# Performance work log

Hardware: AMD Instinct MI355X
Metric: run time of the kernel (lower is better)

Reference implementation:

```python
import jax, jax.numpy as jnp
import numpy as np

E = 8          # node_emb_dim (number of LSTM ensembles)
H = 128        # fixed_lstm_hidden
D = 8          # feature dim
CONT = 168     # cont_len (encoder length)
HORIZON = 24   # decoder length
T = CONT + HORIZON
B = 4096       # batch of node ids
NUM_TS = 4096


def _lstm(xs, W, U, b, h0, c0):
    """Time-major LSTM (Keras gate order i,f,g,o). xs: [T,B,in]. Returns final (h,c) and all hs."""
    def step(carry, x):
        h, c = carry
        z = x @ W + h @ U + b                      # [B, 4H]
        i, f, g, o = jnp.split(z, 4, axis=-1)
        i = jax.nn.sigmoid(i)
        f = jax.nn.sigmoid(f)
        g = jnp.tanh(g)
        o = jax.nn.sigmoid(o)
        c = f * c + i * g
        h = o * jnp.tanh(c)
        return (h, c), h
    (h, c), hs = jax.lax.scan(step, (h0, c0), xs)
    return h, c, hs


def setup_inputs() -> dict:
    key = jax.random.key(0)
    ks = jax.random.split(key, 12)
    s = 0.05  # small init scale to keep LSTM gates unsaturated
    return {
        "feats": jax.random.normal(ks[0], (T, D), jnp.float32),
        "y_prev": jax.random.normal(ks[1], (CONT, B), jnp.float32),
        "nid": jax.random.randint(ks[2], (B,), 0, NUM_TS, jnp.int32),
        "emb_table": jax.random.uniform(ks[3], (NUM_TS, E), jnp.float32),
        "enc_W": jax.random.normal(ks[4], (E, 1 + D, 4 * H), jnp.float32) * s,
        "enc_U": jax.random.normal(ks[5], (E, H, 4 * H), jnp.float32) * s,
        "enc_b": jnp.zeros((E, 4 * H), jnp.float32),
        "dec_W": jax.random.normal(ks[6], (E, D, 4 * H), jnp.float32) * s,
        "dec_U": jax.random.normal(ks[7], (E, H, 4 * H), jnp.float32) * s,
        "dec_b": jnp.zeros((E, 4 * H), jnp.float32),
        "out_w": jax.random.normal(ks[8], (E, H), jnp.float32) * s,
    }


def reference(feats, y_prev, nid, emb_table, enc_W, enc_U, enc_b, dec_W, dec_U, dec_b, out_w):
    cont_len = y_prev.shape[0]
    b = nid.shape[0]
    # normalized node embedding: abs then row-normalize, then lookup
    embs = jnp.abs(emb_table)
    embs = embs / jnp.sum(embs, axis=1, keepdims=True)
    node_emb = embs[nid]                                   # [B, E]
    # broadcast features over batch (time-major)
    feats_b = jnp.broadcast_to(feats[:, None, :], (feats.shape[0], b, feats.shape[1]))
    enc_inp = jnp.concatenate([y_prev[..., None], feats_b[:cont_len]], axis=-1)  # [CONT,B,1+D]
    feats_futr = feats_b[cont_len:]                        # [HOR,B,D]
    hdim = enc_U.shape[1]
    h0 = jnp.zeros((b, hdim), feats.dtype)
    c0 = jnp.zeros((b, hdim), feats.dtype)

    def run_one(eW, eU, eb, dW, dU, db, ow):
        h, c, _ = _lstm(enc_inp, eW, eU, eb, h0, c0)
        _, _, hs = _lstm(feats_futr, dW, dU, db, h, c)     # [HOR,B,H]
        return jnp.einsum('tbh,h->tb', hs, ow)             # Dense(1, no bias) -> [HOR,B]

    outs = jax.vmap(run_one)(enc_W, enc_U, enc_b, dec_W, dec_U, dec_b, out_w)  # [E,HOR,B]
    fixed_effect = jnp.einsum('etb,be->tb', outs, node_emb)                    # [HOR,B]
    return fixed_effect
```

## Files before the change

kernel.cpp:

```cpp
#include <hip/hip_runtime.h>
#include <stdint.h>
#include <type_traits>

#define NE 8
#define NH 128
#define ND 8
#define NCONT 168
#define NHOR 24
#define NB 4096
#define NG 512
#define BT 64

#define S_SIG (-1.44269504088896f)
#define S_TANH (2.88539008177793f)

typedef float f32x4 __attribute__((ext_vector_type(4)));
typedef float f32x2 __attribute__((ext_vector_type(2)));
typedef short bf16x8 __attribute__((ext_vector_type(8)));
typedef unsigned int u32x2 __attribute__((ext_vector_type(2)));

template <int N> using ic = std::integral_constant<int, N>;

__device__ __forceinline__ unsigned short f2bf(float f){
  union { float f; unsigned u; } v; v.f = f;
  unsigned r = (v.u + 0x7FFFu + ((v.u >> 16) & 1u)) >> 16;
  return (unsigned short)r;
}
__device__ __forceinline__ unsigned cvt_pk_bf16(float lo, float hi){
  unsigned r;
  asm("v_cvt_pk_bf16_f32 %0, %1, %2" : "=v"(r) : "v"(lo), "v"(hi));
  return r;
}

__device__ __forceinline__ f32x2 splat2(float v){ f32x2 r; r.x = v; r.y = v; return r; }
__device__ __forceinline__ f32x2 lo2(f32x4 v){ return __builtin_shufflevector(v, v, 0, 1); }
__device__ __forceinline__ f32x2 hi2(f32x4 v){ return __builtin_shufflevector(v, v, 2, 3); }
__device__ __forceinline__ f32x2 fma2(f32x2 a, f32x2 b, f32x2 c){
  return __builtin_elementwise_fma(a, b, c);
}
__device__ __forceinline__ f32x2 exp2_2(f32x2 x){
  f32x2 o; o.x = __builtin_amdgcn_exp2f(x.x); o.y = __builtin_amdgcn_exp2f(x.y); return o;
}
__device__ __forceinline__ f32x2 rcp2(f32x2 x){
  f32x2 o; o.x = __builtin_amdgcn_rcpf(x.x); o.y = __builtin_amdgcn_rcpf(x.y); return o;
}
__device__ __forceinline__ f32x2 gate2(f32x2 zs){
  return rcp2(exp2_2(zs) + splat2(1.0f));
}

__global__ void prep_fxw_enc(const float* __restrict__ feats, const float* __restrict__ W,
                             const float* __restrict__ bias, float* __restrict__ out){
  int idx = blockIdx.x * blockDim.x + threadIdx.x;
  if (idx >= NE * NCONT * NG) return;
  int j = idx & (NG - 1);
  int t = (idx >> 9) % NCONT;
  int e = idx / (NCONT * NG);
  float s = bias[e * NG + j];
  #pragma unroll
  for (int i = 0; i < ND; ++i)
    s += feats[t * ND + i] * W[(e * 9 + 1 + i) * NG + j];
  float sc = ((j >> 7) == 2) ? S_TANH : S_SIG;
  out[idx] = s * sc;
}

__global__ void prep_fxw_dec(const float* __restrict__ feats, const float* __restrict__ W,
                             const float* __restrict__ bias, float* __restrict__ out){
  int idx = blockIdx.x * blockDim.x + threadIdx.x;
  if (idx >= NE * NHOR * NG) return;
  int j = idx & (NG - 1);
  int t = (idx >> 9) % NHOR;
  int e = idx / (NHOR * NG);
  float s = bias[e * NG + j];
  #pragma unroll
  for (int i = 0; i < ND; ++i)
    s += feats[(NCONT + t) * ND + i] * W[(e * ND + i) * NG + j];
  float sc = ((j >> 7) == 2) ? S_TANH : S_SIG;
  out[idx] = s * sc;
}

__global__ void prep_node(const int* __restrict__ nid, const float* __restrict__ emb,
                          float* __restrict__ node_w){
  int b = blockIdx.x * blockDim.x + threadIdx.x;
  if (b >= NB) return;
  int n = nid[b];
  float a[NE]; float s = 0.f;
  #pragma unroll
  for (int e = 0; e < NE; ++e){ a[e] = fabsf(emb[n * NE + e]); s += a[e]; }
  float inv = 1.0f / s;
  #pragma unroll
  for (int e = 0; e < NE; ++e) node_w[b * NE + e] = a[e] * inv;
}

__global__ __launch_bounds__(512, 2) void lstm_main(
    const float* __restrict__ y_prev,
    const float* __restrict__ enc_W,
    const float* __restrict__ enc_U,
    const float* __restrict__ dec_U,
    const float* __restrict__ out_w,
    const float* __restrict__ fxw_enc,
    const float* __restrict__ fxw_dec,
    float* __restrict__ ws_out)
{
  __shared__ unsigned short hl[2][BT * NH];
  __shared__ float part[2][BT][9];

  const int tid  = threadIdx.x;
  const int lane = tid & 63;
  const int w    = tid >> 6;
  const int e    = blockIdx.x & 7;
  const int b0   = (blockIdx.x >> 3) * BT;
  const int l15  = lane & 15;
  const int l4   = lane >> 4;
  const int hc0  = w * 16 + l4 * 4;

  const int q   = (l15 >> 2) & 1;
  const int Ae  = l15 * 128 + ((l4 ^ (l15 & 3)) << 3);
  const int rb0 = 2 * (Ae + q * 32);
  const int rb1 = 2 * (Ae + (1 - q) * 32);
  const int wb  = 2 * ((l15 * 128 + hc0) ^ ((l15 & 7) << 3));

  {
    f32x4 z4 = {0.f, 0.f, 0.f, 0.f};
    ((f32x4*)&hl[0][0])[tid]       = z4;
    ((f32x4*)&hl[0][0])[tid + 512] = z4;
  }

  bf16x8 ut[4][4];
  {
    const float* Ub = enc_U + e * NH * NG + w * 16 + l15;
    #pragma unroll
    for (int g = 0; g < 4; ++g){
      float scg = (g == 2) ? S_TANH : S_SIG;
      #pragma unroll
      for (int kc = 0; kc < 4; ++kc){
        const float* p = Ub + (kc * 32 + l4 * 8) * NG + g * NH;
        bf16x8 v;
        #pragma unroll
        for (int j = 0; j < 8; ++j) v[j] = (short)f2bf(p[j * NG] * scg);
        ut[g][kc] = v;
      }
    }
  }

  f32x2 w042[4][2];
  #pragma unroll
  for (int g = 0; g < 4; ++g){
    float scg = (g == 2) ? S_TANH : S_SIG;
    f32x4 t4 = *(const f32x4*)&enc_W[(e * 9) * NG + g * NH + hc0];
    t4 *= scg;
    w042[g][0] = lo2(t4); w042[g][1] = hi2(t4);
  }

  f32x2 cs2[4][2];
  #pragma unroll
  for (int nf = 0; nf < 4; ++nf){ cs2[nf][0] = splat2(0.f); cs2[nf][1] = splat2(0.f); }

  f32x2 ow2[2];
  f32x4 fxv[4];
  float yv[4];

  const float* fxe = fxw_enc + e * NCONT * NG;
  const float* yp  = y_prev + b0;

  #pragma unroll
  for (int g = 0; g < 4; ++g) fxv[g] = *(const f32x4*)&fxe[g * NH + hc0];
  #pragma unroll
  for (int nf = 0; nf < 4; ++nf) yv[nf] = yp[nf * 16 + l15];

  __syncthreads();

  auto rdnf = [&](auto Bc, auto NFc, bf16x8* hb){
    constexpr int B  = decltype(Bc)::value;
    constexpr int nf = decltype(NFc)::value;
    #pragma unroll
    for (int kc = 0; kc < 4; ++kc)
      hb[kc] = *(const bf16x8*)((const char*)hl +
                 (B * 16384 + nf * 4096 + (kc >> 1) * 128) + ((kc & 1) ? rb1 : rb0));
  };
  auto mmnf = [&](bf16x8* hb, f32x4* ag){
    #pragma unroll
    for (int g = 0; g < 4; ++g)
      ag[g] = __builtin_amdgcn_mfma_f32_16x16x32_bf16(ut[g][0], hb[0], fxv[g], 0, 0, 0);
    #pragma unroll
    for (int kc = 1; kc < 4; ++kc)
      #pragma unroll
      for (int g = 0; g < 4; ++g)
        ag[g] = __builtin_amdgcn_mfma_f32_16x16x32_bf16(ut[g][kc], hb[kc], ag[g], 0, 0, 0);
  };
  auto cellnf = [&](auto Bc, auto ENCc, auto NFc, f32x4* ag, float ycur, float* pout){
    constexpr int  B   = decltype(Bc)::value;
    constexpr bool ENC = decltype(ENCc)::value;
    constexpr int  nf  = decltype(NFc)::value;
    f32x2 h2[2];
    #pragma unroll
    for (int hf = 0; hf < 2; ++hf){
      f32x2 zi = hf ? hi2(ag[0]) : lo2(ag[0]);
      f32x2 zf = hf ? hi2(ag[1]) : lo2(ag[1]);
      f32x2 zg = hf ? hi2(ag[2]) : lo2(ag[2]);
      f32x2 zo = hf ? hi2(ag[3]) : lo2(ag[3]);
      if constexpr (ENC){
        f32x2 y2 = splat2(ycur);
        zi = fma2(y2, w042[0][hf], zi);
        zf = fma2(y2, w042[1][hf], zf);
        zg = fma2(y2, w042[2][hf], zg);
        zo = fma2(y2, w042[3][hf], zo);
      }
      f32x2 gi = gate2(zi);
      f32x2 gf = gate2(zf);
      f32x2 go = gate2(zo);
      f32x2 rg_ = gate2(zg);
      f32x2 gg2 = fma2(rg_, splat2(-2.0f * S_TANH), splat2(S_TANH));
      f32x2 c  = fma2(gf, cs2[nf][hf], gi * gg2);
      cs2[nf][hf] = c;
      f32x2 rc = gate2(c);
      f32x2 th = fma2(rc, splat2(-2.0f), splat2(1.0f));
      h2[hf] = go * th;
    }
    u32x2 pk;
    pk.x = cvt_pk_bf16(h2[0].x, h2[0].y);
    pk.y = cvt_pk_bf16(h2[1].x, h2[1].y);
    *(u32x2*)((char*)hl + ((B ^ 1) * 16384 + nf * 4096) + wb) = pk;
    if constexpr (!ENC){
      f32x2 pp = fma2(h2[0], ow2[0], h2[1] * ow2[1]);
      pout[nf] = pp.x + pp.y;
    }
  };

  auto step = [&](auto Bc, auto ENCc, const float* fxn, const float* ypn, float* pout){
    constexpr bool ENC = decltype(ENCc)::value;

    float ycur[4];
    if constexpr (ENC){
      #pragma unroll
      for (int nf = 0; nf < 4; ++nf) ycur[nf] = yv[nf];
    }

    bf16x8 hbA[4], hbB[4];
    f32x4 a0[4], a1[4], a2[4], a3[4];

    rdnf(Bc, ic<0>{}, hbA); mmnf(hbA, a0);
    rdnf(Bc, ic<1>{}, hbB); mmnf(hbB, a1);
    cellnf(Bc, ENCc, ic<0>{}, a0, ycur[0], pout);
    rdnf(Bc, ic<2>{}, hbA); mmnf(hbA, a2);
    cellnf(Bc, ENCc, ic<1>{}, a1, ycur[1], pout);
    rdnf(Bc, ic<3>{}, hbB); mmnf(hbB, a3);
    #pragma unroll
    for (int g = 0; g < 4; ++g) fxv[g] = *(const f32x4*)&fxn[g * NH + hc0];
    if constexpr (ENC){
      #pragma unroll
      for (int nf = 0; nf < 4; ++nf) yv[nf] = ypn[nf * 16 + l15];
    }
    cellnf(Bc, ENCc, ic<2>{}, a2, ycur[2], pout);
    cellnf(Bc, ENCc, ic<3>{}, a3, ycur[3], pout);
    __syncthreads();
  };

  for (int t = 0; t < NCONT; t += 2){
    step(ic<0>{}, std::true_type{}, fxe + NG, yp + NB, nullptr);
    const float* fx2 = (t + 2 < NCONT) ? fxe + 2 * NG : fxe;
    const float* yp2 = (t + 2 < NCONT) ? yp + 2 * NB  : yp;
    step(ic<1>{}, std::true_type{}, fx2, yp2, nullptr);
    fxe += 2 * NG; yp += 2 * NB;
  }

  {
    const float* Ub = dec_U + e * NH * NG + w * 16 + l15;
    #pragma unroll
    for (int g = 0; g < 4; ++g){
      float scg = (g == 2) ? S_TANH : S_SIG;
      #pragma unroll
      for (int kc = 0; kc < 4; ++kc){
        const float* p = Ub + (kc * 32 + l4 * 8) * NG + g * NH;
        bf16x8 v;
        #pragma unroll
        for (int j = 0; j < 8; ++j) v[j] = (short)f2bf(p[j * NG] * scg);
        ut[g][kc] = v;
      }
    }
  }
  {
    f32x4 ow4 = *(const f32x4*)&out_w[e * NH + hc0];
    ow2[0] = lo2(ow4); ow2[1] = hi2(ow4);
  }

  const float* fxd = fxw_dec + e * NHOR * NG;
  #pragma unroll
  for (int g = 0; g < 4; ++g) fxv[g] = *(const f32x4*)&fxd[g * NH + hc0];

  auto emit = [&](int t, float* pbuf){
    #pragma unroll
    for (int nf = 0; nf < 4; ++nf){
      pbuf[nf] += __shfl_xor(pbuf[nf], 16);
      pbuf[nf] += __shfl_xor(pbuf[nf], 32);
    }
    int pb = t & 1;
    if (lane < 16){
      #pragma unroll
      for (int nf = 0; nf < 4; ++nf) part[pb][nf * 16 + l15][w] = pbuf[nf];
    }
    __syncthreads();
    if (w == 0){
      float s = 0.f;
      #pragma unroll
      for (int ww = 0; ww < 8; ++ww) s += part[pb][lane][ww];
      ws_out[(e * NHOR + t) * NB + b0 + lane] = s;
    }
  };

  #pragma unroll 1
  for (int td = 0; td < NHOR; td += 2){
    float pbuf[4];
    step(ic<0>{}, std::false_type{}, fxd + NG, nullptr, pbuf);
    emit(td, pbuf);
    const float* fx2 = (td + 2 < NHOR) ? fxd + 2 * NG : fxd;
    step(ic<1>{}, std::false_type{}, fx2, nullptr, pbuf);
    emit(td + 1, pbuf);
    fxd += 2 * NG;
  }
}

__global__ void finalize(const float* __restrict__ ws_out, const float* __restrict__ node_w,
                         float* __restrict__ out){
  int idx = blockIdx.x * blockDim.x + threadIdx.x;
  if (idx >= NHOR * NB) return;
  int b = idx & (NB - 1);
  float s = 0.f;
  #pragma unroll
  for (int e = 0; e < NE; ++e)
    s += ws_out[e * NHOR * NB + idx] * node_w[b * NE + e];
  out[idx] = s;
}

extern "C" void kernel_launch(void* const* d_in, const int* in_sizes, int n_in,
                              void* d_out, int out_size, void* d_ws, size_t ws_size,
                              hipStream_t stream) {
  const float* feats  = (const float*)d_in[0];
  const float* y_prev = (const float*)d_in[1];
  const int*   nid    = (const int*)  d_in[2];
  const float* emb    = (const float*)d_in[3];
  const float* enc_W  = (const float*)d_in[4];
  const float* enc_U  = (const float*)d_in[5];
  const float* enc_b  = (const float*)d_in[6];
  const float* dec_W  = (const float*)d_in[7];
  const float* dec_U  = (const float*)d_in[8];
  const float* dec_b  = (const float*)d_in[9];
  const float* out_w  = (const float*)d_in[10];
  float* out = (float*)d_out;

  float* ws      = (float*)d_ws;
  float* fxw_enc = ws;
  float* fxw_dec = fxw_enc + NE * NCONT * NG;
  float* node_w  = fxw_dec + NE * NHOR * NG;
  float* ws_out  = node_w + NB * NE;

  prep_fxw_enc<<<(NE * NCONT * NG + 255) / 256, 256, 0, stream>>>(feats, enc_W, enc_b, fxw_enc);
  prep_fxw_dec<<<(NE * NHOR * NG + 255) / 256, 256, 0, stream>>>(feats, dec_W, dec_b, fxw_dec);
  prep_node<<<(NB + 255) / 256, 256, 0, stream>>>(nid, emb, node_w);
  lstm_main<<<NE * (NB / BT), 512, 0, stream>>>(y_prev, enc_W, enc_U, dec_U, out_w,
                                                fxw_enc, fxw_dec, ws_out);
  finalize<<<(NHOR * NB + 255) / 256, 256, 0, stream>>>(ws_out, node_w, out);
}
```

Measured before the change: 1.100 ms.

## Stage per-step feature projections in LDS and raise occupancy to four blocks

Moves the per-timestep input projection (fxw) and the y-input weights from registers into shared memory, double-buffered, with one cooperative load per thread per step. The interleaved step schedule (two accumulator sets overlapping MFMA with cell math) becomes a simple sequential loop over the four row fragments. Launch bounds change to allow four 512-thread blocks per CU, cutting register pressure to raise occupancy. The trade is less in-wave ILP and extra LDS reads per step.

```diff
diff --git a/kernel.cpp b/kernel.cpp
--- a/kernel.cpp
+++ b/kernel.cpp
@@ -91,7 +91,7 @@
   for (int e = 0; e < NE; ++e) node_w[b * NE + e] = a[e] * inv;
 }
 
-__global__ __launch_bounds__(512, 2) void lstm_main(
+__global__ __launch_bounds__(512, 4) void lstm_main(
     const float* __restrict__ y_prev,
     const float* __restrict__ enc_W,
     const float* __restrict__ enc_U,
@@ -102,6 +102,8 @@
     float* __restrict__ ws_out)
 {
   __shared__ unsigned short hl[2][BT * NH];
+  __shared__ float fxl[2][NG];
+  __shared__ float w04_lds[NG];
   __shared__ float part[2][BT][9];
 
   const int tid  = threadIdx.x;
@@ -119,10 +121,16 @@
   const int rb1 = 2 * (Ae + (1 - q) * 32);
   const int wb  = 2 * ((l15 * 128 + hc0) ^ ((l15 & 7) << 3));
 
+  const float* fxe = fxw_enc + e * NCONT * NG;
+  const float* fxd0 = fxw_dec + e * NHOR * NG;
+
   {
     f32x4 z4 = {0.f, 0.f, 0.f, 0.f};
     ((f32x4*)&hl[0][0])[tid]       = z4;
     ((f32x4*)&hl[0][0])[tid + 512] = z4;
+    float sc = ((tid >> 7) == 2) ? S_TANH : S_SIG;
+    w04_lds[tid] = enc_W[(e * 9) * NG + tid] * sc;
+    fxl[0][tid] = fxe[tid];
   }
 
   bf16x8 ut[4][4];
@@ -142,125 +150,94 @@
     }
   }
 
-  f32x2 w042[4][2];
-  #pragma unroll
-  for (int g = 0; g < 4; ++g){
-    float scg = (g == 2) ? S_TANH : S_SIG;
-    f32x4 t4 = *(const f32x4*)&enc_W[(e * 9) * NG + g * NH + hc0];
-    t4 *= scg;
-    w042[g][0] = lo2(t4); w042[g][1] = hi2(t4);
-  }
-
   f32x2 cs2[4][2];
   #pragma unroll
   for (int nf = 0; nf < 4; ++nf){ cs2[nf][0] = splat2(0.f); cs2[nf][1] = splat2(0.f); }
 
   f32x2 ow2[2];
-  f32x4 fxv[4];
-  float yv[4];
-
-  const float* fxe = fxw_enc + e * NCONT * NG;
-  const float* yp  = y_prev + b0;
-
-  #pragma unroll
-  for (int g = 0; g < 4; ++g) fxv[g] = *(const f32x4*)&fxe[g * NH + hc0];
-  #pragma unroll
-  for (int nf = 0; nf < 4; ++nf) yv[nf] = yp[nf * 16 + l15];
 
   __syncthreads();
 
-  auto rdnf = [&](auto Bc, auto NFc, bf16x8* hb){
-    constexpr int B  = decltype(Bc)::value;
-    constexpr int nf = decltype(NFc)::value;
-    #pragma unroll
-    for (int kc = 0; kc < 4; ++kc)
-      hb[kc] = *(const bf16x8*)((const char*)hl +
-                 (B * 16384 + nf * 4096 + (kc >> 1) * 128) + ((kc & 1) ? rb1 : rb0));
-  };
-  auto mmnf = [&](bf16x8* hb, f32x4* ag){
-    #pragma unroll
-    for (int g = 0; g < 4; ++g)
-      ag[g] = __builtin_amdgcn_mfma_f32_16x16x32_bf16(ut[g][0], hb[0], fxv[g], 0, 0, 0);
-    #pragma unroll
-    for (int kc = 1; kc < 4; ++kc)
-      #pragma unroll
-      for (int g = 0; g < 4; ++g)
-        ag[g] = __builtin_amdgcn_mfma_f32_16x16x32_bf16(ut[g][kc], hb[kc], ag[g], 0, 0, 0);
-  };
-  auto cellnf = [&](auto Bc, auto ENCc, auto NFc, f32x4* ag, float ycur, float* pout){
+  auto step = [&](auto Bc, auto ENCc, const float* fxn, const float* ypt, float* pout){
     constexpr int  B   = decltype(Bc)::value;
     constexpr bool ENC = decltype(ENCc)::value;
-    constexpr int  nf  = decltype(NFc)::value;
-    f32x2 h2[2];
-    #pragma unroll
-    for (int hf = 0; hf < 2; ++hf){
-      f32x2 zi = hf ? hi2(ag[0]) : lo2(ag[0]);
-      f32x2 zf = hf ? hi2(ag[1]) : lo2(ag[1]);
-      f32x2 zg = hf ? hi2(ag[2]) : lo2(ag[2]);
-      f32x2 zo = hf ? hi2(ag[3]) : lo2(ag[3]);
-      if constexpr (ENC){
-        f32x2 y2 = splat2(ycur);
-        zi = fma2(y2, w042[0][hf], zi);
-        zf = fma2(y2, w042[1][hf], zf);
-        zg = fma2(y2, w042[2][hf], zg);
-        zo = fma2(y2, w042[3][hf], zo);
-      }
-      f32x2 gi = gate2(zi);
-      f32x2 gf = gate2(zf);
-      f32x2 go = gate2(zo);
-      f32x2 rg_ = gate2(zg);
-      f32x2 gg2 = fma2(rg_, splat2(-2.0f * S_TANH), splat2(S_TANH));
-      f32x2 c  = fma2(gf, cs2[nf][hf], gi * gg2);
-      cs2[nf][hf] = c;
-      f32x2 rc = gate2(c);
-      f32x2 th = fma2(rc, splat2(-2.0f), splat2(1.0f));
-      h2[hf] = go * th;
-    }
-    u32x2 pk;
-    pk.x = cvt_pk_bf16(h2[0].x, h2[0].y);
-    pk.y = cvt_pk_bf16(h2[1].x, h2[1].y);
-    *(u32x2*)((char*)hl + ((B ^ 1) * 16384 + nf * 4096) + wb) = pk;
-    if constexpr (!ENC){
-      f32x2 pp = fma2(h2[0], ow2[0], h2[1] * ow2[1]);
-      pout[nf] = pp.x + pp.y;
-    }
-  };
-
-  auto step = [&](auto Bc, auto ENCc, const float* fxn, const float* ypn, float* pout){
-    constexpr bool ENC = decltype(ENCc)::value;
-
+
+    float fxst = fxn[tid];
     float ycur[4];
     if constexpr (ENC){
       #pragma unroll
-      for (int nf = 0; nf < 4; ++nf) ycur[nf] = yv[nf];
-    }
-
-    bf16x8 hbA[4], hbB[4];
-    f32x4 a0[4], a1[4], a2[4], a3[4];
-
-    rdnf(Bc, ic<0>{}, hbA); mmnf(hbA, a0);
-    rdnf(Bc, ic<1>{}, hbB); mmnf(hbB, a1);
-    cellnf(Bc, ENCc, ic<0>{}, a0, ycur[0], pout);
-    rdnf(Bc, ic<2>{}, hbA); mmnf(hbA, a2);
-    cellnf(Bc, ENCc, ic<1>{}, a1, ycur[1], pout);
-    rdnf(Bc, ic<3>{}, hbB); mmnf(hbB, a3);
+      for (int nf = 0; nf < 4; ++nf) ycur[nf] = ypt[nf * 16 + l15];
+    }
+
     #pragma unroll
-    for (int g = 0; g < 4; ++g) fxv[g] = *(const f32x4*)&fxn[g * NH + hc0];
-    if constexpr (ENC){
-      #pragma unroll
-      for (int nf = 0; nf < 4; ++nf) yv[nf] = ypn[nf * 16 + l15];
-    }
-    cellnf(Bc, ENCc, ic<2>{}, a2, ycur[2], pout);
-    cellnf(Bc, ENCc, ic<3>{}, a3, ycur[3], pout);
+    for (int nf = 0; nf < 4; ++nf){
+      bf16x8 hb[4];
+      #pragma unroll
+      for (int kc = 0; kc < 4; ++kc)
+        hb[kc] = *(const bf16x8*)((const char*)hl +
+                   (B * 16384 + nf * 4096 + (kc >> 1) * 128) + ((kc & 1) ? rb1 : rb0));
+      f32x4 ag[4];
+      #pragma unroll
+      for (int g = 0; g < 4; ++g){
+        f32x4 fxq = *(const f32x4*)&fxl[B][g * NH + hc0];
+        ag[g] = __builtin_amdgcn_mfma_f32_16x16x32_bf16(ut[g][0], hb[0], fxq, 0, 0, 0);
+      }
+      #pragma unroll
+      for (int kc = 1; kc < 4; ++kc)
+        #pragma unroll
+        for (int g = 0; g < 4; ++g)
+          ag[g] = __builtin_amdgcn_mfma_f32_16x16x32_bf16(ut[g][kc], hb[kc], ag[g], 0, 0, 0);
+
+      f32x2 h2[2];
+      f32x4 w0q[4];
+      if constexpr (ENC){
+        #pragma unroll
+        for (int g = 0; g < 4; ++g) w0q[g] = *(const f32x4*)&w04_lds[g * NH + hc0];
+      }
+      #pragma unroll
+      for (int hf = 0; hf < 2; ++hf){
+        f32x2 zi = hf ? hi2(ag[0]) : lo2(ag[0]);
+        f32x2 zf = hf ? hi2(ag[1]) : lo2(ag[1]);
+        f32x2 zg = hf ? hi2(ag[2]) : lo2(ag[2]);
+        f32x2 zo = hf ? hi2(ag[3]) : lo2(ag[3]);
+        if constexpr (ENC){
+          f32x2 y2 = splat2(ycur[nf]);
+          zi = fma2(y2, hf ? hi2(w0q[0]) : lo2(w0q[0]), zi);
+          zf = fma2(y2, hf ? hi2(w0q[1]) : lo2(w0q[1]), zf);
+          zg = fma2(y2, hf ? hi2(w0q[2]) : lo2(w0q[2]), zg);
+          zo = fma2(y2, hf ? hi2(w0q[3]) : lo2(w0q[3]), zo);
+        }
+        f32x2 gi = gate2(zi);
+        f32x2 gf = gate2(zf);
+        f32x2 go = gate2(zo);
+        f32x2 rg_ = gate2(zg);
+        f32x2 gg2 = fma2(rg_, splat2(-2.0f * S_TANH), splat2(S_TANH));
+        f32x2 c  = fma2(gf, cs2[nf][hf], gi * gg2);
+        cs2[nf][hf] = c;
+        f32x2 rc = gate2(c);
+        f32x2 th = fma2(rc, splat2(-2.0f), splat2(1.0f));
+        h2[hf] = go * th;
+      }
+      u32x2 pk;
+      pk.x = cvt_pk_bf16(h2[0].x, h2[0].y);
+      pk.y = cvt_pk_bf16(h2[1].x, h2[1].y);
+      *(u32x2*)((char*)hl + ((B ^ 1) * 16384 + nf * 4096) + wb) = pk;
+      if constexpr (!ENC){
+        f32x2 pp = fma2(h2[0], ow2[0], h2[1] * ow2[1]);
+        pout[nf] = pp.x + pp.y;
+      }
+    }
+    fxl[B ^ 1][tid] = fxst;
     __syncthreads();
   };
 
+  const float* ypt = y_prev + b0;
   for (int t = 0; t < NCONT; t += 2){
-    step(ic<0>{}, std::true_type{}, fxe + NG, yp + NB, nullptr);
-    const float* fx2 = (t + 2 < NCONT) ? fxe + 2 * NG : fxe;
-    const float* yp2 = (t + 2 < NCONT) ? yp + 2 * NB  : yp;
-    step(ic<1>{}, std::true_type{}, fx2, yp2, nullptr);
-    fxe += 2 * NG; yp += 2 * NB;
+    step(ic<0>{}, std::true_type{}, fxe + NG, ypt, nullptr);
+    ypt += NB;
+    const float* nx = (t + 2 < NCONT) ? fxe + 2 * NG : fxd0;
+    step(ic<1>{}, std::true_type{}, nx, ypt, nullptr);
+    ypt += NB; fxe += 2 * NG;
   }
 
   {
@@ -283,10 +260,6 @@
     ow2[0] = lo2(ow4); ow2[1] = hi2(ow4);
   }
 
-  const float* fxd = fxw_dec + e * NHOR * NG;
-  #pragma unroll
-  for (int g = 0; g < 4; ++g) fxv[g] = *(const f32x4*)&fxd[g * NH + hc0];
-
   auto emit = [&](int t, float* pbuf){
     #pragma unroll
     for (int nf = 0; nf < 4; ++nf){
@@ -307,13 +280,14 @@
     }
   };
 
+  const float* fxd = fxd0;
   #pragma unroll 1
   for (int td = 0; td < NHOR; td += 2){
     float pbuf[4];
     step(ic<0>{}, std::false_type{}, fxd + NG, nullptr, pbuf);
     emit(td, pbuf);
-    const float* fx2 = (td + 2 < NHOR) ? fxd + 2 * NG : fxd;
-    step(ic<1>{}, std::false_type{}, fx2, nullptr, pbuf);
+    const float* nx = (td + 2 < NHOR) ? fxd + 2 * NG : fxd + NG;
+    step(ic<1>{}, std::false_type{}, nx, nullptr, pbuf);
     emit(td + 1, pbuf);
     fxd += 2 * NG;
   }
```

After: 4.050 ms. +268.2%, slower.
